# Performance work log

Hardware: AMD Instinct MI355X
Metric: run time of the kernel (lower is better)

The kernel has to match this reference:

```python
import jax, jax.numpy as jnp
import numpy as np

N = 50000          # points
K = 16             # neighbors per query (n_max)
M = N * K          # ragged pair count
DIM = 96
HEADS = 6
HEAD_DIM = DIM // HEADS
WINDOW = 4.0
QUANT = 0.25
QGL = int(WINDOW / QUANT)   # quant_grid_length = 16
SCALE = HEAD_DIM ** -0.5


def setup_inputs() -> dict:
    key = jax.random.key(0)
    ks = jax.random.split(key, 10)
    feats = jax.random.normal(ks[0], (N, DIM), dtype=jnp.float32)
    xyz = jax.random.uniform(ks[1], (N, 3), dtype=jnp.float32) * 8.0
    index_0 = jnp.repeat(jnp.arange(N, dtype=jnp.int32), K)            # sorted query ids
    index_1 = jax.random.randint(ks[2], (M,), 0, N, dtype=jnp.int32)   # neighbor ids
    index_0_offsets = jnp.arange(N + 1, dtype=jnp.int32) * K
    W_qkv = jax.random.normal(ks[3], (DIM, 3 * DIM), dtype=jnp.float32) * 0.02
    b_qkv = jnp.zeros((3 * DIM,), dtype=jnp.float32)
    table_q = jax.random.normal(ks[4], (4 * QGL, HEADS, HEAD_DIM, 3), dtype=jnp.float32) * 0.02
    table_k = jax.random.normal(ks[5], (4 * QGL, HEADS, HEAD_DIM, 3), dtype=jnp.float32) * 0.02
    table_v = jax.random.normal(ks[6], (4 * QGL, HEADS, HEAD_DIM, 3), dtype=jnp.float32) * 0.02
    W_proj = jax.random.normal(ks[7], (DIM, DIM), dtype=jnp.float32) * 0.02
    b_proj = jnp.zeros((DIM,), dtype=jnp.float32)
    return {
        "feats": feats, "xyz": xyz,
        "index_0": index_0, "index_0_offsets": index_0_offsets, "n_max": K,
        "index_1": index_1, "shift_size": jnp.float32(0.0),
        "W_qkv": W_qkv, "b_qkv": b_qkv,
        "table_q": table_q, "table_k": table_k, "table_v": table_v,
        "W_proj": W_proj, "b_proj": b_proj,
    }


def reference(feats, xyz, index_0, index_0_offsets, n_max, index_1, shift_size,
              W_qkv, b_qkv, table_q, table_k, table_v, W_proj, b_proj):
    n = feats.shape[0]
    # qkv projection -> (N, 3, H, HD)
    qkv = (feats @ W_qkv + b_qkv).reshape(n, 3, HEADS, HEAD_DIM)
    q = qkv[:, 0] * SCALE
    k = qkv[:, 1]
    v = qkv[:, 2]

    # step1: per-pair QK dot product (pointops.attention_step1_v2)
    qg = q[index_0]                      # (M, H, HD) gathered by query id
    kg = k[index_1]                      # (M, H, HD) gathered by neighbor id
    attn = jnp.einsum('mhd,mhd->mh', qg, kg)   # (M, H)

    # quantized relative positions
    xyz_quant = jnp.floor(((xyz - xyz.min(axis=0) + shift_size) % WINDOW) / QUANT)
    rel = xyz_quant[index_0] - xyz_quant[index_1]       # (M, 3)
    rel_idx = (rel + (QGL - 1)).astype(jnp.int32)       # map_func, in [0, 2*QGL-2]

    # relative position bias (pointops.dot_prod_with_idx_v3: query + key tables)
    bias = jnp.zeros_like(attn)
    for c in range(3):   # fixed 3 coordinate axes
        tq = table_q[rel_idx[:, c], :, :, c]            # (M, H, HD)
        tk = table_k[rel_idx[:, c], :, :, c]
        bias = bias + jnp.einsum('mhd,mhd->mh', qg, tq) + jnp.einsum('mhd,mhd->mh', kg, tk)
    attn = attn + bias

    # scatter softmax over index_0 segments
    seg_max = jax.ops.segment_max(attn, index_0, num_segments=n)
    e = jnp.exp(attn - seg_max[index_0])
    denom = jax.ops.segment_sum(e, index_0, num_segments=n)
    sm = e / denom[index_0]                              # (M, H)

    # step2 with relative position value (pointops.attention_step2_with_rel_pos_value_v2)
    vg = v[index_1]                                      # (M, H, HD)
    for c in range(3):
        vg = vg + table_v[rel_idx[:, c], :, :, c]
    x = jax.ops.segment_sum(sm[:, :, None] * vg, index_0, num_segments=n)  # (N, H, HD)
    x = x.reshape(n, DIM)
    return x @ W_proj + b_proj
```

## Files before the change

### kernel.cpp

```cpp
#include <hip/hip_runtime.h>
#include <hip/hip_fp16.h>
#include <math.h>

#define FLT_BIG 3.402823466e38f
typedef unsigned int uint;
typedef unsigned short ushort;
typedef __attribute__((ext_vector_type(8))) _Float16 half8;
typedef __attribute__((ext_vector_type(4))) float floatx4;

__device__ inline ushort f2h(float f) {
    return __half_as_ushort(__float2half(f));
}
__device__ inline float dot2(uint a, uint b, float c) {
    float d;
    asm("v_dot2_f32_f16 %0, %1, %2, %3" : "=v"(d) : "v"(a), "v"(b), "v"(c));
    return d;
}
template <int CTRL>
__device__ inline float dppf(float x) {
    return __int_as_float(__builtin_amdgcn_update_dpp(
        __float_as_int(x), __float_as_int(x), CTRL, 0xF, 0xF, true));
}

__global__ void min_reduce_kernel(const float* __restrict__ xyz, int n, float* mn) {
    float m0 = FLT_BIG, m1 = FLT_BIG, m2 = FLT_BIG;
    for (int i = blockIdx.x * blockDim.x + threadIdx.x; i < n; i += gridDim.x * blockDim.x) {
        m0 = fminf(m0, xyz[3 * i + 0]);
        m1 = fminf(m1, xyz[3 * i + 1]);
        m2 = fminf(m2, xyz[3 * i + 2]);
    }
#pragma unroll
    for (int off = 32; off > 0; off >>= 1) {
        m0 = fminf(m0, __shfl_down(m0, off));
        m1 = fminf(m1, __shfl_down(m1, off));
        m2 = fminf(m2, __shfl_down(m2, off));
    }
    if ((threadIdx.x & 63) == 0) {
        atomicMin((int*)&mn[0], __float_as_int(m0));
        atomicMin((int*)&mn[1], __float_as_int(m1));
        atomicMin((int*)&mn[2], __float_as_int(m2));
    }
}

__global__ void prep_kernel(const float* __restrict__ W_qkv,
                            const float* __restrict__ W_proj,
                            const float* __restrict__ tq, const float* __restrict__ tk,
                            const float* __restrict__ tv,
                            ushort* __restrict__ wtqkv, ushort* __restrict__ wtproj,
                            ushort* __restrict__ rq, ushort* __restrict__ rk,
                            ushort* __restrict__ rv, float* mn) {
    int tid = blockIdx.x * 256 + threadIdx.x;
    if (tid < 3) mn[tid] = FLT_BIG;
    if (tid < 18432) {
        int c = tid / 6144, rem = tid - c * 6144;
        int idx = rem / 96, hd = rem - idx * 96;
        int src = (idx * 96 + hd) * 3 + c;
        rq[tid] = f2h(tq[src]);
        rk[tid] = f2h(tk[src]);
        rv[tid] = f2h(tv[src]);
    }
    if (tid < 27648) {
        int j = tid / 96, d = tid - j * 96;
        wtqkv[tid] = f2h(W_qkv[d * 288 + j]);
    }
    if (tid < 9216) {
        int j = tid / 96, d = tid - j * 96;
        wtproj[tid] = f2h(W_proj[d * 96 + j]);
    }
}

__global__ __launch_bounds__(384) void qkv_mfma_kernel(
    const float* __restrict__ A, const ushort* __restrict__ WT,
    const float* __restrict__ bias, uint4* __restrict__ qout4,
    uint4* __restrict__ kvout4, const float* __restrict__ xyz,
    const float* __restrict__ mn, const float* __restrict__ shiftp,
    uint* __restrict__ xq, int n) {
    __shared__ ushort Ash[64 * 104];
    __shared__ ushort lds[6][32 * 112];
    const int t = threadIdx.x;
    const int row0 = blockIdx.x * 64;

    if (t < 64) {
        int rp = row0 + t;
        if (rp < n) {
            float shift = shiftp[0];
            float q0 = floorf(fmodf(xyz[3 * rp + 0] - mn[0] + shift, 4.0f) * 4.0f);
            float q1 = floorf(fmodf(xyz[3 * rp + 1] - mn[1] + shift, 4.0f) * 4.0f);
            float q2 = floorf(fmodf(xyz[3 * rp + 2] - mn[2] + shift, 4.0f) * 4.0f);
            xq[rp] = (uint)(int)q0 | ((uint)(int)q1 << 8) | ((uint)(int)q2 << 16);
        }
    }

    const float4* A4 = (const float4*)A;
#pragma unroll
    for (int j = 0; j < 4; j++) {
        int idx = t + j * 384;
        int row = idx / 24, c4 = idx - row * 24;
        int gr = row0 + row; if (gr > n - 1) gr = n - 1;
        float4 v = A4[(size_t)gr * 24 + c4];
        uint2 pk;
        pk.x = (uint)f2h(v.x) | ((uint)f2h(v.y) << 16);
        pk.y = (uint)f2h(v.z) | ((uint)f2h(v.w) << 16);
        *(uint2*)&Ash[row * 104 + c4 * 4] = pk;
    }
    __syncthreads();

    const int wave = t >> 6, lane = t & 63;
    const int ch = wave >> 1, rg = wave & 1;
    const int m = lane & 15, q = lane >> 4;
    const int wrow0 = row0 + rg * 32;

    const ushort* wbase = WT + ((size_t)ch * 96 + m) * 96 + q * 8;

    floatx4 acc[2][6];
#pragma unroll
    for (int g = 0; g < 2; g++)
#pragma unroll
        for (int ct = 0; ct < 6; ct++) acc[g][ct] = (floatx4){0.f, 0.f, 0.f, 0.f};

#pragma unroll
    for (int kk4 = 0; kk4 < 24; kk4 += 8) {
        half8 a0 = *(const half8*)&Ash[(rg * 32 + m) * 104 + (kk4 + q * 2) * 4];
        half8 a1 = *(const half8*)&Ash[(rg * 32 + 16 + m) * 104 + (kk4 + q * 2) * 4];
#pragma unroll
        for (int ct = 0; ct < 6; ct++) {
            half8 b = *(const half8*)(wbase + ct * 16 * 96 + kk4 * 4);
            acc[0][ct] = __builtin_amdgcn_mfma_f32_16x16x32_f16(a0, b, acc[0][ct], 0, 0, 0);
            acc[1][ct] = __builtin_amdgcn_mfma_f32_16x16x32_f16(a1, b, acc[1][ct], 0, 0, 0);
        }
    }

    ushort* L = lds[wave];
    const float sc = (ch == 0) ? 0.25f : 1.0f;
#pragma unroll
    for (int g = 0; g < 2; g++)
#pragma unroll
        for (int ct = 0; ct < 6; ct++) {
            float bv = bias[ch * 96 + ct * 16 + m];
#pragma unroll
            for (int r = 0; r < 4; r++) {
                int rowl = g * 16 + q * 4 + r;
                L[rowl * 112 + ct * 16 + m] = f2h((acc[g][ct][r] + bv) * sc);
            }
        }
    const int strideU4 = (ch == 0) ? 12 : 24;
    const int offU4 = (ch == 2) ? 12 : 0;
    uint4* dst = (ch == 0) ? qout4 : kvout4;
#pragma unroll
    for (int i = 0; i < 6; i++) {
        int idx = i * 64 + lane;
        int rowl = idx / 12, u4 = idx - rowl * 12;
        int grow = wrow0 + rowl;
        if (grow < n) {
            uint4 val = *(const uint4*)(L + rowl * 112 + u4 * 8);
            dst[(size_t)grow * strideU4 + offU4 + u4] = val;
        }
    }
}

__global__ __launch_bounds__(256) void proj_mfma_kernel(
    const ushort* __restrict__ A, const ushort* __restrict__ WT,
    const float* __restrict__ bias, float* __restrict__ out, int n) {
    const int wave = threadIdx.x >> 6, lane = threadIdx.x & 63;
    const int m = lane & 15, q = lane >> 4;
    const int row0 = blockIdx.x * 128 + wave * 32;
    if (row0 >= n) return;

    const ushort* wbase = WT + (size_t)m * 96 + q * 8;
    int r0 = row0 + m;      if (r0 > n - 1) r0 = n - 1;
    int r1 = row0 + 16 + m; if (r1 > n - 1) r1 = n - 1;

    floatx4 acc[2][6];
#pragma unroll
    for (int g = 0; g < 2; g++)
#pragma unroll
        for (int ct = 0; ct < 6; ct++) acc[g][ct] = (floatx4){0.f, 0.f, 0.f, 0.f};

#pragma unroll
    for (int kk = 0; kk < 96; kk += 32) {
        half8 a0 = *(const half8*)(A + (size_t)r0 * 96 + q * 8 + kk);
        half8 a1 = *(const half8*)(A + (size_t)r1 * 96 + q * 8 + kk);
#pragma unroll
        for (int ct = 0; ct < 6; ct++) {
            half8 b = *(const half8*)(wbase + ct * 16 * 96 + kk);
            acc[0][ct] = __builtin_amdgcn_mfma_f32_16x16x32_f16(a0, b, acc[0][ct], 0, 0, 0);
            acc[1][ct] = __builtin_amdgcn_mfma_f32_16x16x32_f16(a1, b, acc[1][ct], 0, 0, 0);
        }
    }

#pragma unroll
    for (int g = 0; g < 2; g++)
#pragma unroll
        for (int ct = 0; ct < 6; ct++) {
            int col = ct * 16 + m;
            float bv = bias[col];
#pragma unroll
            for (int r = 0; r < 4; r++) {
                int row = row0 + g * 16 + q * 4 + r;
                if (row < n) out[(size_t)row * 96 + col] = acc[g][ct][r] + bv;
            }
        }
}

#define ATTN_NB 256
#define ATTN_B 8
#define TPITCH 208
#define TSIZE  39936
__global__ __launch_bounds__(768) void attn_kernel(
    const ushort* __restrict__ qh, const ushort* __restrict__ kv,
    const uint* __restrict__ xq, const int* __restrict__ index_1,
    const ushort* __restrict__ rq, const ushort* __restrict__ rk,
    const ushort* __restrict__ rv, ushort* __restrict__ xout, int n) {
    __shared__ uint4 ldsraw[7488];
    char* Lb = (char*)ldsraw;

    const int t = threadIdx.x;
    const int pt = t / 96, tp = t - pt * 96;
    const int h = tp >> 4, e = tp & 15;

    const int stride = gridDim.x * ATTN_B;
    const int iters = (n + stride - 1) / stride;

    int pA, jdA; uint xqpA;
    auto PREF_A = [&](int it) {
        pA = (it * gridDim.x + blockIdx.x) * ATTN_B + pt;
        int pc = pA < n ? pA : n - 1;
        jdA = index_1[(size_t)pc * 16 + e];
        xqpA = xq[pc];
    };
    int p, jd; uint xqp, xqj;
    uint4 ka, kb, va, vb, qa, qb;
    auto PREF_B = [&]() {
        p = pA; jd = jdA; xqp = xqpA;
        int pc = p < n ? p : n - 1;
        const ushort* row = kv + (size_t)jd * 192;
        ka = *(const uint4*)(row + h * 16);
        kb = *(const uint4*)(row + h * 16 + 8);
        va = *(const uint4*)(row + 96 + h * 16);
        vb = *(const uint4*)(row + 96 + h * 16 + 8);
        const ushort* qrow = qh + (size_t)pc * 96 + h * 16;
        qa = *(const uint4*)qrow;
        qb = *(const uint4*)(qrow + 8);
        xqj = xq[jd];
    };
    PREF_A(0); PREF_B(); PREF_A(1);

#pragma unroll
    for (int j = 0; j < 9; j++) {
        const uint4* src = (j < 3) ? (const uint4*)rq
                         : (j < 6) ? (const uint4*)rk : (const uint4*)rv;
        int rem = t + (j % 3) * 768;
        int ROW = rem / 12, slot = rem - ROW * 12;
        uint4 val = src[rem];
        *(uint4*)(Lb + (j / 3) * TSIZE + ROW * TPITCH + slot * 16) = val;
    }
    __syncthreads();

    auto LD2 = [&](const char* base, int R, uint4& A, uint4& B) {
        const char* rb = base + R * TPITCH + h * 32;
        A = *(const uint4*)rb;
        B = *(const uint4*)(rb + 16);
    };
    auto F2 = [](const uint4& u, int i) -> float2 {
        return __half22float2(((const __half2*)&u)[i]);
    };

    const bool b3 = (e & 8) != 0, b2 = (e & 4) != 0;
    const bool b1 = (e & 2) != 0, b0 = (e & 1) != 0;

    for (int it = 0; it < iters; it++) {
        const int i0 = (int)(xqp & 255u) - (int)(xqj & 255u) + 15;
        const int i1 = (int)((xqp >> 8) & 255u) - (int)((xqj >> 8) & 255u) + 15;
        const int i2 = (int)((xqp >> 16) & 255u) - (int)((xqj >> 16) & 255u) + 15;

        float f[16];
#pragma unroll
        for (int i = 0; i < 4; i++) {
            float2 lo = F2(va, i), hi = F2(vb, i);
            f[2 * i] = lo.x; f[2 * i + 1] = lo.y;
            f[8 + 2 * i] = hi.x; f[8 + 2 * i + 1] = hi.y;
        }

        float a;
        {
            float x0 = dot2(qa.x, ka.x, 0.f), x1 = dot2(qa.y, ka.y, 0.f);
            x0 = dot2(qa.z, ka.z, x0); x1 = dot2(qa.w, ka.w, x1);
            x0 = dot2(qb.x, kb.x, x0); x1 = dot2(qb.y, kb.y, x1);
            x0 = dot2(qb.z, kb.z, x0); x1 = dot2(qb.w, kb.w, x1);
            float bias = 0.f;
#define BIAS_C(ROW)                                                            \
            {                                                                  \
                uint4 ta, tb, ua, ub;                                          \
                LD2(Lb, (ROW), ta, tb);                                        \
                LD2(Lb + TSIZE, (ROW), ua, ub);                                \
                float u = dot2(qa.x, ta.x, 0.f), w = dot2(ka.x, ua.x, 0.f);    \
                u = dot2(qa.y, ta.y, u); w = dot2(ka.y, ua.y, w);              \
                u = dot2(qa.z, ta.z, u); w = dot2(ka.z, ua.z, w);              \
                u = dot2(qa.w, ta.w, u); w = dot2(ka.w, ua.w, w);              \
                u = dot2(qb.x, tb.x, u); w = dot2(kb.x, ub.x, w);              \
                u = dot2(qb.y, tb.y, u); w = dot2(kb.y, ub.y, w);              \
                u = dot2(qb.z, tb.z, u); w = dot2(kb.z, ub.z, w);              \
                u = dot2(qb.w, tb.w, u); w = dot2(kb.w, ub.w, w);              \
                bias += u + w;                                                 \
            }
            BIAS_C(i0)
            BIAS_C(64 + i1)
            BIAS_C(128 + i2)
#undef BIAS_C
            a = x0 + x1 + bias;
        }

        const int op = p;
        if (it + 1 < iters) { PREF_B(); PREF_A(it + 2); }

        {
            uint4 t0a, t0b, t1a, t1b, t2a, t2b;
            LD2(Lb + 2 * TSIZE, i0, t0a, t0b);
            LD2(Lb + 2 * TSIZE, 64 + i1, t1a, t1b);
            LD2(Lb + 2 * TSIZE, 128 + i2, t2a, t2b);
#pragma unroll
            for (int i = 0; i < 4; i++) {
                float2 a0 = F2(t0a, i), a1 = F2(t1a, i), a2 = F2(t2a, i);
                f[2 * i]     += a0.x + a1.x + a2.x;
                f[2 * i + 1] += a0.y + a1.y + a2.y;
                float2 c0 = F2(t0b, i), c1 = F2(t1b, i), c2 = F2(t2b, i);
                f[8 + 2 * i]     += c0.x + c1.x + c2.x;
                f[8 + 2 * i + 1] += c0.y + c1.y + c2.y;
            }
        }

        float wgt;
        {
            float mx = a;
            mx = fmaxf(mx, dppf<0x128>(mx));
            mx = fmaxf(mx, dppf<0x124>(mx));
            mx = fmaxf(mx, dppf<0x122>(mx));
            mx = fmaxf(mx, dppf<0x121>(mx));
            float ex = __expf(a - mx);
            float sum = ex;
            sum += dppf<0x128>(sum);
            sum += dppf<0x124>(sum);
            sum += dppf<0x122>(sum);
            sum += dppf<0x121>(sum);
            wgt = ex * __builtin_amdgcn_rcpf(sum);
        }

        float P[16];
#pragma unroll
        for (int c = 0; c < 16; c++) P[c] = wgt * f[c];
        float A8[8];
#pragma unroll
        for (int j = 0; j < 8; j++) {
            float kp = b3 ? P[j + 8] : P[j];
            float sd = b3 ? P[j] : P[j + 8];
            A8[j] = kp + dppf<0x140>(sd);
        }
        float B4[4];
#pragma unroll
        for (int j = 0; j < 4; j++) {
            float kp = b2 ? A8[j + 4] : A8[j];
            float sd = b2 ? A8[j] : A8[j + 4];
            B4[j] = kp + dppf<0x141>(sd);
        }
        float C2[2];
#pragma unroll
        for (int j = 0; j < 2; j++) {
            float kp = b1 ? B4[j + 2] : B4[j];
            float sd = b1 ? B4[j] : B4[j + 2];
            C2[j] = kp + dppf<0x4E>(sd);
        }
        {
            float kp = b0 ? C2[1] : C2[0];
            float sd = b0 ? C2[0] : C2[1];
            float xres = kp + dppf<0xB1>(sd);
            if (op < n) xout[(size_t)op * 96 + tp] = f2h(xres);
        }
    }
}

extern "C" void kernel_launch(void* const* d_in, const int* in_sizes, int n_in,
                              void* d_out, int out_size, void* d_ws, size_t ws_size,
                              hipStream_t stream) {
    const float* feats   = (const float*)d_in[0];
    const float* xyz     = (const float*)d_in[1];
    const int*   index_1 = (const int*)d_in[5];
    const float* shiftp  = (const float*)d_in[6];
    const float* W_qkv   = (const float*)d_in[7];
    const float* b_qkv   = (const float*)d_in[8];
    const float* table_q = (const float*)d_in[9];
    const float* table_k = (const float*)d_in[10];
    const float* table_v = (const float*)d_in[11];
    const float* W_proj  = (const float*)d_in[12];
    const float* b_proj  = (const float*)d_in[13];
    float* out = (float*)d_out;

    const int n = in_sizes[0] / 96;

    float* w = (float*)d_ws;
    float*  mn     = w;
    ushort* qbf    = (ushort*)(w + 16);
    ushort* kvbuf  = qbf + (size_t)n * 96;
    ushort* xbuf   = kvbuf + (size_t)n * 192;
    ushort* wtqkv  = xbuf + (size_t)n * 96;
    ushort* wtproj = wtqkv + 27648;
    ushort* rq     = wtproj + 9216;
    ushort* rk     = rq + 18432;
    ushort* rv     = rk + 18432;
    uint*   xqv    = (uint*)(rv + 18432);

    prep_kernel<<<108, 256, 0, stream>>>(W_qkv, W_proj, table_q, table_k, table_v,
                                         wtqkv, wtproj, rq, rk, rv, mn);
    min_reduce_kernel<<<256, 256, 0, stream>>>(xyz, n, mn);
    qkv_mfma_kernel<<<(n + 63) / 64, 384, 0, stream>>>(feats, wtqkv, b_qkv,
                                                       (uint4*)qbf, (uint4*)kvbuf,
                                                       xyz, mn, shiftp, xqv, n);
    attn_kernel<<<ATTN_NB, 768, 0, stream>>>(qbf, kvbuf, xqv, index_1, rq, rk,
                                             rv, xbuf, n);
    proj_mfma_kernel<<<(n + 127) / 128, 256, 0, stream>>>(xbuf, wtproj, b_proj,
                                                          out, n);
}
```

Baseline: 225.6 us.

## Fuse all stages into one persistent cooperative kernel with grid syncs

Merges the weight/table preparation, coordinate min-reduction, QKV GEMM, attention and output projection into a single cooperative kernel of 256 blocks with 768 threads, separated by grid.sync barriers. The min-reduce now uses per-block partials plus a second-pass reduction instead of global atomics, and the QKV GEMM loops over 128-row tiles persistently. This removes four kernel launch gaps and the atomic contention. In exchange it adds grid-wide barriers and forces the GEMM phases to run at the attention kernel's occupancy and shared-memory footprint.

```diff
diff --git a/kernel.cpp b/kernel.cpp
--- a/kernel.cpp
+++ b/kernel.cpp
@@ -1,6 +1,9 @@
 #include <hip/hip_runtime.h>
+#include <hip/hip_cooperative_groups.h>
 #include <hip/hip_fp16.h>
 #include <math.h>
+
+namespace cg = cooperative_groups;
 
 #define FLT_BIG 3.402823466e38f
 typedef unsigned int uint;
@@ -22,358 +25,375 @@
         __float_as_int(x), __float_as_int(x), CTRL, 0xF, 0xF, true));
 }
 
-__global__ void min_reduce_kernel(const float* __restrict__ xyz, int n, float* mn) {
-    float m0 = FLT_BIG, m1 = FLT_BIG, m2 = FLT_BIG;
-    for (int i = blockIdx.x * blockDim.x + threadIdx.x; i < n; i += gridDim.x * blockDim.x) {
-        m0 = fminf(m0, xyz[3 * i + 0]);
-        m1 = fminf(m1, xyz[3 * i + 1]);
-        m2 = fminf(m2, xyz[3 * i + 2]);
-    }
-#pragma unroll
-    for (int off = 32; off > 0; off >>= 1) {
-        m0 = fminf(m0, __shfl_down(m0, off));
-        m1 = fminf(m1, __shfl_down(m1, off));
-        m2 = fminf(m2, __shfl_down(m2, off));
-    }
-    if ((threadIdx.x & 63) == 0) {
-        atomicMin((int*)&mn[0], __float_as_int(m0));
-        atomicMin((int*)&mn[1], __float_as_int(m1));
-        atomicMin((int*)&mn[2], __float_as_int(m2));
-    }
-}
-
-__global__ void prep_kernel(const float* __restrict__ W_qkv,
-                            const float* __restrict__ W_proj,
-                            const float* __restrict__ tq, const float* __restrict__ tk,
-                            const float* __restrict__ tv,
-                            ushort* __restrict__ wtqkv, ushort* __restrict__ wtproj,
-                            ushort* __restrict__ rq, ushort* __restrict__ rk,
-                            ushort* __restrict__ rv, float* mn) {
-    int tid = blockIdx.x * 256 + threadIdx.x;
-    if (tid < 3) mn[tid] = FLT_BIG;
-    if (tid < 18432) {
-        int c = tid / 6144, rem = tid - c * 6144;
-        int idx = rem / 96, hd = rem - idx * 96;
-        int src = (idx * 96 + hd) * 3 + c;
-        rq[tid] = f2h(tq[src]);
-        rk[tid] = f2h(tk[src]);
-        rv[tid] = f2h(tv[src]);
-    }
-    if (tid < 27648) {
-        int j = tid / 96, d = tid - j * 96;
-        wtqkv[tid] = f2h(W_qkv[d * 288 + j]);
-    }
-    if (tid < 9216) {
-        int j = tid / 96, d = tid - j * 96;
-        wtproj[tid] = f2h(W_proj[d * 96 + j]);
-    }
-}
-
-__global__ __launch_bounds__(384) void qkv_mfma_kernel(
-    const float* __restrict__ A, const ushort* __restrict__ WT,
-    const float* __restrict__ bias, uint4* __restrict__ qout4,
-    uint4* __restrict__ kvout4, const float* __restrict__ xyz,
-    const float* __restrict__ mn, const float* __restrict__ shiftp,
-    uint* __restrict__ xq, int n) {
-    __shared__ ushort Ash[64 * 104];
-    __shared__ ushort lds[6][32 * 112];
-    const int t = threadIdx.x;
-    const int row0 = blockIdx.x * 64;
-
-    if (t < 64) {
-        int rp = row0 + t;
-        if (rp < n) {
-            float shift = shiftp[0];
-            float q0 = floorf(fmodf(xyz[3 * rp + 0] - mn[0] + shift, 4.0f) * 4.0f);
-            float q1 = floorf(fmodf(xyz[3 * rp + 1] - mn[1] + shift, 4.0f) * 4.0f);
-            float q2 = floorf(fmodf(xyz[3 * rp + 2] - mn[2] + shift, 4.0f) * 4.0f);
-            xq[rp] = (uint)(int)q0 | ((uint)(int)q1 << 8) | ((uint)(int)q2 << 16);
-        }
-    }
-
-    const float4* A4 = (const float4*)A;
-#pragma unroll
-    for (int j = 0; j < 4; j++) {
-        int idx = t + j * 384;
-        int row = idx / 24, c4 = idx - row * 24;
-        int gr = row0 + row; if (gr > n - 1) gr = n - 1;
-        float4 v = A4[(size_t)gr * 24 + c4];
-        uint2 pk;
-        pk.x = (uint)f2h(v.x) | ((uint)f2h(v.y) << 16);
-        pk.y = (uint)f2h(v.z) | ((uint)f2h(v.w) << 16);
-        *(uint2*)&Ash[row * 104 + c4 * 4] = pk;
-    }
-    __syncthreads();
-
-    const int wave = t >> 6, lane = t & 63;
-    const int ch = wave >> 1, rg = wave & 1;
-    const int m = lane & 15, q = lane >> 4;
-    const int wrow0 = row0 + rg * 32;
-
-    const ushort* wbase = WT + ((size_t)ch * 96 + m) * 96 + q * 8;
-
-    floatx4 acc[2][6];
-#pragma unroll
-    for (int g = 0; g < 2; g++)
-#pragma unroll
-        for (int ct = 0; ct < 6; ct++) acc[g][ct] = (floatx4){0.f, 0.f, 0.f, 0.f};
-
-#pragma unroll
-    for (int kk4 = 0; kk4 < 24; kk4 += 8) {
-        half8 a0 = *(const half8*)&Ash[(rg * 32 + m) * 104 + (kk4 + q * 2) * 4];
-        half8 a1 = *(const half8*)&Ash[(rg * 32 + 16 + m) * 104 + (kk4 + q * 2) * 4];
-#pragma unroll
-        for (int ct = 0; ct < 6; ct++) {
-            half8 b = *(const half8*)(wbase + ct * 16 * 96 + kk4 * 4);
-            acc[0][ct] = __builtin_amdgcn_mfma_f32_16x16x32_f16(a0, b, acc[0][ct], 0, 0, 0);
-            acc[1][ct] = __builtin_amdgcn_mfma_f32_16x16x32_f16(a1, b, acc[1][ct], 0, 0, 0);
-        }
-    }
-
-    ushort* L = lds[wave];
-    const float sc = (ch == 0) ? 0.25f : 1.0f;
-#pragma unroll
-    for (int g = 0; g < 2; g++)
-#pragma unroll
-        for (int ct = 0; ct < 6; ct++) {
-            float bv = bias[ch * 96 + ct * 16 + m];
-#pragma unroll
-            for (int r = 0; r < 4; r++) {
-                int rowl = g * 16 + q * 4 + r;
-                L[rowl * 112 + ct * 16 + m] = f2h((acc[g][ct][r] + bv) * sc);
-            }
-        }
-    const int strideU4 = (ch == 0) ? 12 : 24;
-    const int offU4 = (ch == 2) ? 12 : 0;
-    uint4* dst = (ch == 0) ? qout4 : kvout4;
-#pragma unroll
-    for (int i = 0; i < 6; i++) {
-        int idx = i * 64 + lane;
-        int rowl = idx / 12, u4 = idx - rowl * 12;
-        int grow = wrow0 + rowl;
-        if (grow < n) {
-            uint4 val = *(const uint4*)(L + rowl * 112 + u4 * 8);
-            dst[(size_t)grow * strideU4 + offU4 + u4] = val;
-        }
-    }
-}
-
-__global__ __launch_bounds__(256) void proj_mfma_kernel(
-    const ushort* __restrict__ A, const ushort* __restrict__ WT,
-    const float* __restrict__ bias, float* __restrict__ out, int n) {
-    const int wave = threadIdx.x >> 6, lane = threadIdx.x & 63;
-    const int m = lane & 15, q = lane >> 4;
-    const int row0 = blockIdx.x * 128 + wave * 32;
-    if (row0 >= n) return;
-
-    const ushort* wbase = WT + (size_t)m * 96 + q * 8;
-    int r0 = row0 + m;      if (r0 > n - 1) r0 = n - 1;
-    int r1 = row0 + 16 + m; if (r1 > n - 1) r1 = n - 1;
-
-    floatx4 acc[2][6];
-#pragma unroll
-    for (int g = 0; g < 2; g++)
-#pragma unroll
-        for (int ct = 0; ct < 6; ct++) acc[g][ct] = (floatx4){0.f, 0.f, 0.f, 0.f};
-
-#pragma unroll
-    for (int kk = 0; kk < 96; kk += 32) {
-        half8 a0 = *(const half8*)(A + (size_t)r0 * 96 + q * 8 + kk);
-        half8 a1 = *(const half8*)(A + (size_t)r1 * 96 + q * 8 + kk);
-#pragma unroll
-        for (int ct = 0; ct < 6; ct++) {
-            half8 b = *(const half8*)(wbase + ct * 16 * 96 + kk);
-            acc[0][ct] = __builtin_amdgcn_mfma_f32_16x16x32_f16(a0, b, acc[0][ct], 0, 0, 0);
-            acc[1][ct] = __builtin_amdgcn_mfma_f32_16x16x32_f16(a1, b, acc[1][ct], 0, 0, 0);
-        }
-    }
-
-#pragma unroll
-    for (int g = 0; g < 2; g++)
-#pragma unroll
-        for (int ct = 0; ct < 6; ct++) {
-            int col = ct * 16 + m;
-            float bv = bias[col];
-#pragma unroll
-            for (int r = 0; r < 4; r++) {
-                int row = row0 + g * 16 + q * 4 + r;
-                if (row < n) out[(size_t)row * 96 + col] = acc[g][ct][r] + bv;
-            }
-        }
-}
-
-#define ATTN_NB 256
+#define NBLK 256
+#define NTHR 768
 #define ATTN_B 8
 #define TPITCH 208
 #define TSIZE  39936
-__global__ __launch_bounds__(768) void attn_kernel(
-    const ushort* __restrict__ qh, const ushort* __restrict__ kv,
-    const uint* __restrict__ xq, const int* __restrict__ index_1,
-    const ushort* __restrict__ rq, const ushort* __restrict__ rk,
-    const ushort* __restrict__ rv, ushort* __restrict__ xout, int n) {
-    __shared__ uint4 ldsraw[7488];
-    char* Lb = (char*)ldsraw;
-
-    const int t = threadIdx.x;
-    const int pt = t / 96, tp = t - pt * 96;
-    const int h = tp >> 4, e = tp & 15;
-
-    const int stride = gridDim.x * ATTN_B;
-    const int iters = (n + stride - 1) / stride;
-
-    int pA, jdA; uint xqpA;
-    auto PREF_A = [&](int it) {
-        pA = (it * gridDim.x + blockIdx.x) * ATTN_B + pt;
-        int pc = pA < n ? pA : n - 1;
-        jdA = index_1[(size_t)pc * 16 + e];
-        xqpA = xq[pc];
-    };
-    int p, jd; uint xqp, xqj;
-    uint4 ka, kb, va, vb, qa, qb;
-    auto PREF_B = [&]() {
-        p = pA; jd = jdA; xqp = xqpA;
-        int pc = p < n ? p : n - 1;
-        const ushort* row = kv + (size_t)jd * 192;
-        ka = *(const uint4*)(row + h * 16);
-        kb = *(const uint4*)(row + h * 16 + 8);
-        va = *(const uint4*)(row + 96 + h * 16);
-        vb = *(const uint4*)(row + 96 + h * 16 + 8);
-        const ushort* qrow = qh + (size_t)pc * 96 + h * 16;
-        qa = *(const uint4*)qrow;
-        qb = *(const uint4*)(qrow + 8);
-        xqj = xq[jd];
-    };
-    PREF_A(0); PREF_B(); PREF_A(1);
-
-#pragma unroll
-    for (int j = 0; j < 9; j++) {
-        const uint4* src = (j < 3) ? (const uint4*)rq
-                         : (j < 6) ? (const uint4*)rk : (const uint4*)rv;
-        int rem = t + (j % 3) * 768;
-        int ROW = rem / 12, slot = rem - ROW * 12;
-        uint4 val = src[rem];
-        *(uint4*)(Lb + (j / 3) * TSIZE + ROW * TPITCH + slot * 16) = val;
+
+__global__ __launch_bounds__(NTHR) void fused_kernel(
+    const float* __restrict__ feats, const float* __restrict__ xyz,
+    const int* __restrict__ index_1, const float* __restrict__ shiftp,
+    const float* __restrict__ W_qkv, const float* __restrict__ b_qkv,
+    const float* __restrict__ tq, const float* __restrict__ tk,
+    const float* __restrict__ tv,
+    const float* __restrict__ W_proj, const float* __restrict__ b_proj,
+    float* __restrict__ out,
+    ushort* __restrict__ qbf, ushort* __restrict__ kvbuf,
+    ushort* __restrict__ xbuf,
+    ushort* __restrict__ wtqkv, ushort* __restrict__ wtproj,
+    ushort* __restrict__ rq, ushort* __restrict__ rk, ushort* __restrict__ rv,
+    uint* __restrict__ xq, float* __restrict__ pmin, int n) {
+
+    __shared__ __align__(16) char smem[119808];
+    cg::grid_group grid = cg::this_grid();
+    const int t = threadIdx.x, b = blockIdx.x;
+    const int gtid = b * NTHR + t;
+
+    if (gtid < 18432) {
+        int c = gtid / 6144, rem = gtid - c * 6144;
+        int idx = rem / 96, hd = rem - idx * 96;
+        int src = (idx * 96 + hd) * 3 + c;
+        rq[gtid] = f2h(tq[src]);
+        rk[gtid] = f2h(tk[src]);
+        rv[gtid] = f2h(tv[src]);
+    }
+    if (gtid < 27648) {
+        int j = gtid / 96, d = gtid - j * 96;
+        wtqkv[gtid] = f2h(W_qkv[d * 288 + j]);
+    }
+    if (gtid < 9216) {
+        int j = gtid / 96, d = gtid - j * 96;
+        wtproj[gtid] = f2h(W_proj[d * 96 + j]);
+    }
+    {
+        float m0 = FLT_BIG, m1 = FLT_BIG, m2 = FLT_BIG;
+        for (int i = gtid; i < n; i += NBLK * NTHR) {
+            m0 = fminf(m0, xyz[3 * i + 0]);
+            m1 = fminf(m1, xyz[3 * i + 1]);
+            m2 = fminf(m2, xyz[3 * i + 2]);
+        }
+#pragma unroll
+        for (int off = 32; off > 0; off >>= 1) {
+            m0 = fminf(m0, __shfl_down(m0, off));
+            m1 = fminf(m1, __shfl_down(m1, off));
+            m2 = fminf(m2, __shfl_down(m2, off));
+        }
+        float* red = (float*)smem;
+        if ((t & 63) == 0) {
+            red[(t >> 6) * 3 + 0] = m0;
+            red[(t >> 6) * 3 + 1] = m1;
+            red[(t >> 6) * 3 + 2] = m2;
+        }
+        __syncthreads();
+        if (t < 3) {
+            float mm = red[t];
+#pragma unroll
+            for (int wv = 1; wv < 12; wv++) mm = fminf(mm, red[wv * 3 + t]);
+            pmin[b * 3 + t] = mm;
+        }
+    }
+    grid.sync();
+
+    float* mnv = (float*)(smem + 119792);
+    {
+        const int wv = t >> 6, ln = t & 63;
+        if (wv < 3) {
+            float mm = FLT_BIG;
+            for (int k = ln; k < NBLK; k += 64) mm = fminf(mm, pmin[k * 3 + wv]);
+#pragma unroll
+            for (int off = 32; off > 0; off >>= 1) mm = fminf(mm, __shfl_down(mm, off));
+            if (ln == 0) mnv[wv] = mm;
+        }
     }
     __syncthreads();
-
-    auto LD2 = [&](const char* base, int R, uint4& A, uint4& B) {
-        const char* rb = base + R * TPITCH + h * 32;
-        A = *(const uint4*)rb;
-        B = *(const uint4*)(rb + 16);
-    };
-    auto F2 = [](const uint4& u, int i) -> float2 {
-        return __half22float2(((const __half2*)&u)[i]);
-    };
-
-    const bool b3 = (e & 8) != 0, b2 = (e & 4) != 0;
-    const bool b1 = (e & 2) != 0, b0 = (e & 1) != 0;
-
-    for (int it = 0; it < iters; it++) {
-        const int i0 = (int)(xqp & 255u) - (int)(xqj & 255u) + 15;
-        const int i1 = (int)((xqp >> 8) & 255u) - (int)((xqj >> 8) & 255u) + 15;
-        const int i2 = (int)((xqp >> 16) & 255u) - (int)((xqj >> 16) & 255u) + 15;
-
-        float f[16];
-#pragma unroll
-        for (int i = 0; i < 4; i++) {
-            float2 lo = F2(va, i), hi = F2(vb, i);
-            f[2 * i] = lo.x; f[2 * i + 1] = lo.y;
-            f[8 + 2 * i] = hi.x; f[8 + 2 * i + 1] = hi.y;
-        }
-
-        float a;
-        {
-            float x0 = dot2(qa.x, ka.x, 0.f), x1 = dot2(qa.y, ka.y, 0.f);
-            x0 = dot2(qa.z, ka.z, x0); x1 = dot2(qa.w, ka.w, x1);
-            x0 = dot2(qb.x, kb.x, x0); x1 = dot2(qb.y, kb.y, x1);
-            x0 = dot2(qb.z, kb.z, x0); x1 = dot2(qb.w, kb.w, x1);
-            float bias = 0.f;
+    {
+        const float mn0 = mnv[0], mn1 = mnv[1], mn2 = mnv[2];
+        const float shift = shiftp[0];
+        ushort* Ash = (ushort*)smem;
+        ushort* eplds = (ushort*)(smem + 26624);
+        const int wave = t >> 6, lane = t & 63;
+        const int ch = wave >> 2, rg = wave & 3;
+        const int m = lane & 15, q = lane >> 4;
+        const float4* A4 = (const float4*)feats;
+        const ushort* wbase = wtqkv + ((size_t)ch * 96 + m) * 96 + q * 8;
+        const int ntile = (n + 127) >> 7;
+
+        for (int tile = b; tile < ntile; tile += NBLK) {
+            const int row0 = tile << 7;
+            __syncthreads();
+            if (t < 128) {
+                int rp = row0 + t;
+                if (rp < n) {
+                    float q0 = floorf(fmodf(xyz[3 * rp + 0] - mn0 + shift, 4.0f) * 4.0f);
+                    float q1 = floorf(fmodf(xyz[3 * rp + 1] - mn1 + shift, 4.0f) * 4.0f);
+                    float q2 = floorf(fmodf(xyz[3 * rp + 2] - mn2 + shift, 4.0f) * 4.0f);
+                    xq[rp] = (uint)(int)q0 | ((uint)(int)q1 << 8) | ((uint)(int)q2 << 16);
+                }
+            }
+#pragma unroll
+            for (int j = 0; j < 4; j++) {
+                int idx = t + j * NTHR;
+                int row = idx / 24, c4 = idx - row * 24;
+                int gr = row0 + row; if (gr > n - 1) gr = n - 1;
+                float4 v = A4[(size_t)gr * 24 + c4];
+                uint2 pk;
+                pk.x = (uint)f2h(v.x) | ((uint)f2h(v.y) << 16);
+                pk.y = (uint)f2h(v.z) | ((uint)f2h(v.w) << 16);
+                *(uint2*)&Ash[row * 104 + c4 * 4] = pk;
+            }
+            __syncthreads();
+
+            floatx4 acc[2][6];
+#pragma unroll
+            for (int g = 0; g < 2; g++)
+#pragma unroll
+                for (int ct = 0; ct < 6; ct++) acc[g][ct] = (floatx4){0.f, 0.f, 0.f, 0.f};
+#pragma unroll
+            for (int kk4 = 0; kk4 < 24; kk4 += 8) {
+                half8 a0 = *(const half8*)&Ash[(rg * 32 + m) * 104 + (kk4 + q * 2) * 4];
+                half8 a1 = *(const half8*)&Ash[(rg * 32 + 16 + m) * 104 + (kk4 + q * 2) * 4];
+#pragma unroll
+                for (int ct = 0; ct < 6; ct++) {
+                    half8 bb = *(const half8*)(wbase + ct * 16 * 96 + kk4 * 4);
+                    acc[0][ct] = __builtin_amdgcn_mfma_f32_16x16x32_f16(a0, bb, acc[0][ct], 0, 0, 0);
+                    acc[1][ct] = __builtin_amdgcn_mfma_f32_16x16x32_f16(a1, bb, acc[1][ct], 0, 0, 0);
+                }
+            }
+
+            ushort* L = eplds + wave * 3584;
+            const float sc = (ch == 0) ? 0.25f : 1.0f;
+#pragma unroll
+            for (int g = 0; g < 2; g++)
+#pragma unroll
+                for (int ct = 0; ct < 6; ct++) {
+                    float bv = b_qkv[ch * 96 + ct * 16 + m];
+#pragma unroll
+                    for (int r = 0; r < 4; r++) {
+                        int rowl = g * 16 + q * 4 + r;
+                        L[rowl * 112 + ct * 16 + m] = f2h((acc[g][ct][r] + bv) * sc);
+                    }
+                }
+            const int wrow0 = row0 + rg * 32;
+            const int strideU4 = (ch == 0) ? 12 : 24;
+            const int offU4 = (ch == 2) ? 12 : 0;
+            uint4* dst = (ch == 0) ? (uint4*)qbf : (uint4*)kvbuf;
+#pragma unroll
+            for (int i = 0; i < 6; i++) {
+                int idx = i * 64 + lane;
+                int rowl = idx / 12, u4 = idx - rowl * 12;
+                int grow = wrow0 + rowl;
+                if (grow < n) {
+                    uint4 val = *(const uint4*)(L + rowl * 112 + u4 * 8);
+                    dst[(size_t)grow * strideU4 + offU4 + u4] = val;
+                }
+            }
+        }
+    }
+    grid.sync();
+
+    {
+        char* Lb = smem;
+        const int pt = t / 96, tp = t - pt * 96;
+        const int h = tp >> 4, e = tp & 15;
+        const int stride = NBLK * ATTN_B;
+        const int iters = (n + stride - 1) / stride;
+
+        int pA, jdA; uint xqpA;
+        auto PREF_A = [&](int it) {
+            pA = (it * NBLK + b) * ATTN_B + pt;
+            int pc = pA < n ? pA : n - 1;
+            jdA = index_1[(size_t)pc * 16 + e];
+            xqpA = xq[pc];
+        };
+        int p, jd; uint xqp, xqj;
+        uint4 ka, kb, va, vb, qa, qb;
+        auto PREF_B = [&]() {
+            p = pA; jd = jdA; xqp = xqpA;
+            int pc = p < n ? p : n - 1;
+            const ushort* row = kvbuf + (size_t)jd * 192;
+            ka = *(const uint4*)(row + h * 16);
+            kb = *(const uint4*)(row + h * 16 + 8);
+            va = *(const uint4*)(row + 96 + h * 16);
+            vb = *(const uint4*)(row + 96 + h * 16 + 8);
+            const ushort* qrow = qbf + (size_t)pc * 96 + h * 16;
+            qa = *(const uint4*)qrow;
+            qb = *(const uint4*)(qrow + 8);
+            xqj = xq[jd];
+        };
+        PREF_A(0); PREF_B(); PREF_A(1);
+
+#pragma unroll
+        for (int j = 0; j < 9; j++) {
+            const uint4* src = (j < 3) ? (const uint4*)rq
+                             : (j < 6) ? (const uint4*)rk : (const uint4*)rv;
+            int rem = t + (j % 3) * NTHR;
+            int ROW = rem / 12, slot = rem - ROW * 12;
+            uint4 val = src[rem];
+            *(uint4*)(Lb + (j / 3) * TSIZE + ROW * TPITCH + slot * 16) = val;
+        }
+        __syncthreads();
+
+        auto LD2 = [&](const char* base, int R, uint4& A, uint4& B) {
+            const char* rb = base + R * TPITCH + h * 32;
+            A = *(const uint4*)rb;
+            B = *(const uint4*)(rb + 16);
+        };
+        auto F2 = [](const uint4& u, int i) -> float2 {
+            return __half22float2(((const __half2*)&u)[i]);
+        };
+
+        const bool b3 = (e & 8) != 0, b2 = (e & 4) != 0;
+        const bool b1 = (e & 2) != 0, b0 = (e & 1) != 0;
+
+        for (int it = 0; it < iters; it++) {
+            const int i0 = (int)(xqp & 255u) - (int)(xqj & 255u) + 15;
+            const int i1 = (int)((xqp >> 8) & 255u) - (int)((xqj >> 8) & 255u) + 15;
+            const int i2 = (int)((xqp >> 16) & 255u) - (int)((xqj >> 16) & 255u) + 15;
+
+            float f[16];
+#pragma unroll
+            for (int i = 0; i < 4; i++) {
+                float2 lo = F2(va, i), hi = F2(vb, i);
+                f[2 * i] = lo.x; f[2 * i + 1] = lo.y;
+                f[8 + 2 * i] = hi.x; f[8 + 2 * i + 1] = hi.y;
+            }
+
+            float a;
+            {
+                float x0 = dot2(qa.x, ka.x, 0.f), x1 = dot2(qa.y, ka.y, 0.f);
+                x0 = dot2(qa.z, ka.z, x0); x1 = dot2(qa.w, ka.w, x1);
+                x0 = dot2(qb.x, kb.x, x0); x1 = dot2(qb.y, kb.y, x1);
+                x0 = dot2(qb.z, kb.z, x0); x1 = dot2(qb.w, kb.w, x1);
+                float bias = 0.f;
 #define BIAS_C(ROW)                                                            \
-            {                                                                  \
-                uint4 ta, tb, ua, ub;                                          \
-                LD2(Lb, (ROW), ta, tb);                                        \
-                LD2(Lb + TSIZE, (ROW), ua, ub);                                \
-                float u = dot2(qa.x, ta.x, 0.f), w = dot2(ka.x, ua.x, 0.f);    \
-                u = dot2(qa.y, ta.y, u); w = dot2(ka.y, ua.y, w);              \
-                u = dot2(qa.z, ta.z, u); w = dot2(ka.z, ua.z, w);              \
-                u = dot2(qa.w, ta.w, u); w = dot2(ka.w, ua.w, w);              \
-                u = dot2(qb.x, tb.x, u); w = dot2(kb.x, ub.x, w);              \
-                u = dot2(qb.y, tb.y, u); w = dot2(kb.y, ub.y, w);              \
-                u = dot2(qb.z, tb.z, u); w = dot2(kb.z, ub.z, w);              \
-                u = dot2(qb.w, tb.w, u); w = dot2(kb.w, ub.w, w);              \
-                bias += u + w;                                                 \
-            }
-            BIAS_C(i0)
-            BIAS_C(64 + i1)
-            BIAS_C(128 + i2)
+                {                                                              \
+                    uint4 ta, tb, ua, ub;                                      \
+                    LD2(Lb, (ROW), ta, tb);                                    \
+                    LD2(Lb + TSIZE, (ROW), ua, ub);                            \
+                    float u = dot2(qa.x, ta.x, 0.f), w = dot2(ka.x, ua.x, 0.f);\
+                    u = dot2(qa.y, ta.y, u); w = dot2(ka.y, ua.y, w);          \
+                    u = dot2(qa.z, ta.z, u); w = dot2(ka.z, ua.z, w);          \
+                    u = dot2(qa.w, ta.w, u); w = dot2(ka.w, ua.w, w);          \
+                    u = dot2(qb.x, tb.x, u); w = dot2(kb.x, ub.x, w);          \
+                    u = dot2(qb.y, tb.y, u); w = dot2(kb.y, ub.y, w);          \
+                    u = dot2(qb.z, tb.z, u); w = dot2(kb.z, ub.z, w);          \
+                    u = dot2(qb.w, tb.w, u); w = dot2(kb.w, ub.w, w);          \
+                    bias += u + w;                                             \
+                }
+                BIAS_C(i0)
+                BIAS_C(64 + i1)
+                BIAS_C(128 + i2)
 #undef BIAS_C
-            a = x0 + x1 + bias;
-        }
-
-        const int op = p;
-        if (it + 1 < iters) { PREF_B(); PREF_A(it + 2); }
-
-        {
-            uint4 t0a, t0b, t1a, t1b, t2a, t2b;
-            LD2(Lb + 2 * TSIZE, i0, t0a, t0b);
-            LD2(Lb + 2 * TSIZE, 64 + i1, t1a, t1b);
-            LD2(Lb + 2 * TSIZE, 128 + i2, t2a, t2b);
-#pragma unroll
-            for (int i = 0; i < 4; i++) {
-                float2 a0 = F2(t0a, i), a1 = F2(t1a, i), a2 = F2(t2a, i);
-                f[2 * i]     += a0.x + a1.x + a2.x;
-                f[2 * i + 1] += a0.y + a1.y + a2.y;
-                float2 c0 = F2(t0b, i), c1 = F2(t1b, i), c2 = F2(t2b, i);
-                f[8 + 2 * i]     += c0.x + c1.x + c2.x;
-                f[8 + 2 * i + 1] += c0.y + c1.y + c2.y;
-            }
-        }
-
-        float wgt;
-        {
-            float mx = a;
-            mx = fmaxf(mx, dppf<0x128>(mx));
-            mx = fmaxf(mx, dppf<0x124>(mx));
-            mx = fmaxf(mx, dppf<0x122>(mx));
-            mx = fmaxf(mx, dppf<0x121>(mx));
-            float ex = __expf(a - mx);
-            float sum = ex;
-            sum += dppf<0x128>(sum);
-            sum += dppf<0x124>(sum);
-            sum += dppf<0x122>(sum);
-            sum += dppf<0x121>(sum);
-            wgt = ex * __builtin_amdgcn_rcpf(sum);
-        }
-
-        float P[16];
-#pragma unroll
-        for (int c = 0; c < 16; c++) P[c] = wgt * f[c];
-        float A8[8];
-#pragma unroll
-        for (int j = 0; j < 8; j++) {
-            float kp = b3 ? P[j + 8] : P[j];
-            float sd = b3 ? P[j] : P[j + 8];
-            A8[j] = kp + dppf<0x140>(sd);
-        }
-        float B4[4];
-#pragma unroll
-        for (int j = 0; j < 4; j++) {
-            float kp = b2 ? A8[j + 4] : A8[j];
-            float sd = b2 ? A8[j] : A8[j + 4];
-            B4[j] = kp + dppf<0x141>(sd);
-        }
-        float C2[2];
-#pragma unroll
-        for (int j = 0; j < 2; j++) {
-            float kp = b1 ? B4[j + 2] : B4[j];
-            float sd = b1 ? B4[j] : B4[j + 2];
-            C2[j] = kp + dppf<0x4E>(sd);
-        }
-        {
-            float kp = b0 ? C2[1] : C2[0];
-            float sd = b0 ? C2[0] : C2[1];
-            float xres = kp + dppf<0xB1>(sd);
-            if (op < n) xout[(size_t)op * 96 + tp] = f2h(xres);
+                a = x0 + x1 + bias;
+            }
+
+            const int op = p;
+            if (it + 1 < iters) { PREF_B(); PREF_A(it + 2); }
+
+            {
+                uint4 t0a, t0b, t1a, t1b, t2a, t2b;
+                LD2(Lb + 2 * TSIZE, i0, t0a, t0b);
+                LD2(Lb + 2 * TSIZE, 64 + i1, t1a, t1b);
+                LD2(Lb + 2 * TSIZE, 128 + i2, t2a, t2b);
+#pragma unroll
+                for (int i = 0; i < 4; i++) {
+                    float2 a0 = F2(t0a, i), a1 = F2(t1a, i), a2 = F2(t2a, i);
+                    f[2 * i]     += a0.x + a1.x + a2.x;
+                    f[2 * i + 1] += a0.y + a1.y + a2.y;
+                    float2 c0 = F2(t0b, i), c1 = F2(t1b, i), c2 = F2(t2b, i);
+                    f[8 + 2 * i]     += c0.x + c1.x + c2.x;
+                    f[8 + 2 * i + 1] += c0.y + c1.y + c2.y;
+                }
+            }
+
+            float wgt;
+            {
+                float mx = a;
+                mx = fmaxf(mx, dppf<0x128>(mx));
+                mx = fmaxf(mx, dppf<0x124>(mx));
+                mx = fmaxf(mx, dppf<0x122>(mx));
+                mx = fmaxf(mx, dppf<0x121>(mx));
+                float ex = __expf(a - mx);
+                float sum = ex;
+                sum += dppf<0x128>(sum);
+                sum += dppf<0x124>(sum);
+                sum += dppf<0x122>(sum);
+                sum += dppf<0x121>(sum);
+                wgt = ex * __builtin_amdgcn_rcpf(sum);
+            }
+
+            float P[16];
+#pragma unroll
+            for (int c = 0; c < 16; c++) P[c] = wgt * f[c];
+            float A8[8];
+#pragma unroll
+            for (int j = 0; j < 8; j++) {
+                float kp = b3 ? P[j + 8] : P[j];
+                float sd = b3 ? P[j] : P[j + 8];
+                A8[j] = kp + dppf<0x140>(sd);
+            }
+            float B4[4];
+#pragma unroll
+            for (int j = 0; j < 4; j++) {
+                float kp = b2 ? A8[j + 4] : A8[j];
+                float sd = b2 ? A8[j] : A8[j + 4];
+                B4[j] = kp + dppf<0x141>(sd);
+            }
+            float C2[2];
+#pragma unroll
+            for (int j = 0; j < 2; j++) {
+                float kp = b1 ? B4[j + 2] : B4[j];
+                float sd = b1 ? B4[j] : B4[j + 2];
+                C2[j] = kp + dppf<0x4E>(sd);
+            }
+            {
+                float kp = b0 ? C2[1] : C2[0];
+                float sd = b0 ? C2[0] : C2[1];
+                float xres = kp + dppf<0xB1>(sd);
+                if (op < n) xbuf[(size_t)op * 96 + tp] = f2h(xres);
+            }
+        }
+    }
+    grid.sync();
+
+    {
+        const int wave = t >> 6, lane = t & 63;
+        const int m = lane & 15, q = lane >> 4;
+        const int job = b * 12 + wave;
+        const int row0 = job * 32;
+        if (row0 < n) {
+            const ushort* wbase = wtproj + (size_t)m * 96 + q * 8;
+            int r0 = row0 + m;      if (r0 > n - 1) r0 = n - 1;
+            int r1 = row0 + 16 + m; if (r1 > n - 1) r1 = n - 1;
+            floatx4 acc[2][6];
+#pragma unroll
+            for (int g = 0; g < 2; g++)
+#pragma unroll
+                for (int ct = 0; ct < 6; ct++) acc[g][ct] = (floatx4){0.f, 0.f, 0.f, 0.f};
+#pragma unroll
+            for (int kk = 0; kk < 96; kk += 32) {
+                half8 a0 = *(const half8*)(xbuf + (size_t)r0 * 96 + q * 8 + kk);
+                half8 a1 = *(const half8*)(xbuf + (size_t)r1 * 96 + q * 8 + kk);
+#pragma unroll
+                for (int ct = 0; ct < 6; ct++) {
+                    half8 bb = *(const half8*)(wbase + ct * 16 * 96 + kk);
+                    acc[0][ct] = __builtin_amdgcn_mfma_f32_16x16x32_f16(a0, bb, acc[0][ct], 0, 0, 0);
+                    acc[1][ct] = __builtin_amdgcn_mfma_f32_16x16x32_f16(a1, bb, acc[1][ct], 0, 0, 0);
+                }
+            }
+#pragma unroll
+            for (int g = 0; g < 2; g++)
+#pragma unroll
+                for (int ct = 0; ct < 6; ct++) {
+                    int col = ct * 16 + m;
+                    float bv = b_proj[col];
+#pragma unroll
+                    for (int r = 0; r < 4; r++) {
+                        int row = row0 + g * 16 + q * 4 + r;
+                        if (row < n) out[(size_t)row * 96 + col] = acc[g][ct][r] + bv;
+                    }
+                }
         }
     }
 }
@@ -394,11 +414,11 @@
     const float* b_proj  = (const float*)d_in[13];
     float* out = (float*)d_out;
 
-    const int n = in_sizes[0] / 96;
+    int n = in_sizes[0] / 96;
 
     float* w = (float*)d_ws;
-    float*  mn     = w;
-    ushort* qbf    = (ushort*)(w + 16);
+    float*  pmin   = w;
+    ushort* qbf    = (ushort*)(w + 768);
     ushort* kvbuf  = qbf + (size_t)n * 96;
     ushort* xbuf   = kvbuf + (size_t)n * 192;
     ushort* wtqkv  = xbuf + (size_t)n * 96;
@@ -408,14 +428,14 @@
     ushort* rv     = rk + 18432;
     uint*   xqv    = (uint*)(rv + 18432);
 
-    prep_kernel<<<108, 256, 0, stream>>>(W_qkv, W_proj, table_q, table_k, table_v,
-                                         wtqkv, wtproj, rq, rk, rv, mn);
-    min_reduce_kernel<<<256, 256, 0, stream>>>(xyz, n, mn);
-    qkv_mfma_kernel<<<(n + 63) / 64, 384, 0, stream>>>(feats, wtqkv, b_qkv,
-                                                       (uint4*)qbf, (uint4*)kvbuf,
-                                                       xyz, mn, shiftp, xqv, n);
-    attn_kernel<<<ATTN_NB, 768, 0, stream>>>(qbf, kvbuf, xqv, index_1, rq, rk,
-                                             rv, xbuf, n);
-    proj_mfma_kernel<<<(n + 127) / 128, 256, 0, stream>>>(xbuf, wtproj, b_proj,
-                                                          out, n);
+    void* args[] = {
+        (void*)&feats, (void*)&xyz, (void*)&index_1, (void*)&shiftp,
+        (void*)&W_qkv, (void*)&b_qkv, (void*)&table_q, (void*)&table_k,
+        (void*)&table_v, (void*)&W_proj, (void*)&b_proj, (void*)&out,
+        (void*)&qbf, (void*)&kvbuf, (void*)&xbuf, (void*)&wtqkv,
+        (void*)&wtproj, (void*)&rq, (void*)&rk, (void*)&rv,
+        (void*)&xqv, (void*)&pmin, (void*)&n,
+    };
+    hipLaunchCooperativeKernel((const void*)fused_kernel, dim3(NBLK), dim3(NTHR),
+                               args, 0, stream);
 }
```

Result: slower. 285.5 us (+26.5%).
